# Performance work log

Measured on AMD Instinct MI355X. Metric: run time of the kernel, lower is better.

## Reference

```python
import jax, jax.numpy as jnp
import numpy as np

N = 262144
C = 4096  # number of clusters


def _segment_max(x, seg, num_segments):
    # global_max_pool: per-cluster max over points
    return jax.ops.segment_max(x, seg, num_segments=num_segments)


def setup_inputs() -> dict:
    key = jax.random.key(0)
    ks = jax.random.split(key, 16)

    def lin(k, fan_in, fan_out):
        bound = 1.0 / np.sqrt(fan_in)
        kw, kb = jax.random.split(k)
        W = jax.random.uniform(kw, (fan_in, fan_out), jnp.float32, -bound, bound)
        b = jax.random.uniform(kb, (fan_out,), jnp.float32, -bound, bound)
        return W, b

    relative_points = jax.random.normal(ks[0], (N, 3), jnp.float32)
    features = jax.random.normal(ks[1], (N, 64), jnp.float32)
    cluster = jax.random.randint(ks[2], (N,), 0, C, jnp.int64)

    enc_W1, enc_b1 = lin(ks[3], 3, 32)    # neighborhood encoder MLP
    enc_W2, enc_b2 = lin(ks[4], 32, 64)
    W1, b1 = lin(ks[5], 3 + 64 + 64, 128)  # fc_layers (input_size + enc_out + 3)
    W2, b2 = lin(ks[6], 128, 128)
    G1, gb1 = lin(ks[7], 128, 128)          # fc_layers_global
    G2, gb2 = lin(ks[8], 128, 256)

    return dict(relative_points=relative_points, features=features, cluster=cluster,
                enc_W1=enc_W1, enc_b1=enc_b1, enc_W2=enc_W2, enc_b2=enc_b2,
                W1=W1, b1=b1, W2=W2, b2=b2, G1=G1, gb1=gb1, G2=G2, gb2=gb2)


def reference(relative_points, features, cluster,
              enc_W1, enc_b1, enc_W2, enc_b2,
              W1, b1, W2, b2, G1, gb1, G2, gb2):
    # --- neighborhood encoder: per-point MLP then per-cluster max-pool ---
    h = jax.nn.relu(relative_points @ enc_W1 + enc_b1)          # [N, 32]
    h = jax.nn.relu(h @ enc_W2 + enc_b2)                        # [N, 64]
    neigh_enc = _segment_max(h, cluster, C)                     # [C, 64]

    # gather-by-index duplication + concat
    dup = neigh_enc[cluster]                                    # [N, 64]
    encoded = jnp.concatenate([relative_points, features, dup], axis=1)  # [N, 131]

    # local fc stack (relu, leaky=False)
    encoded = jax.nn.relu(encoded @ W1 + b1)                    # [N, 128]
    encoded = jax.nn.relu(encoded @ W2 + b2)                    # [N, 128]

    # global_max_pool (mean=False)
    encoded_global = _segment_max(encoded, cluster, C)          # [C, 128]

    # global fc stack
    encoded_global = jax.nn.relu(encoded_global @ G1 + gb1)     # [C, 128]
    encoded_global = jax.nn.relu(encoded_global @ G2 + gb2)     # [C, 256]
    return encoded_global
```

## Files before the change

kernel.cpp:

```cpp
#include <hip/hip_runtime.h>
#include <hip/hip_bf16.h>

#define NN 262144
#define CC 4096
#define NBLK 128
#define PPB (NN / NBLK)
#define NT (NN / 64)
#define SLOTS 3

typedef __attribute__((ext_vector_type(8))) short bf16x8;
typedef __attribute__((ext_vector_type(4))) float f32x4;

__device__ __forceinline__ unsigned pk2(float a, float b) {
  __hip_bfloat16 ha = __float2bfloat16(a);
  __hip_bfloat16 hb = __float2bfloat16(b);
  unsigned short ua, ub;
  __builtin_memcpy(&ua, &ha, 2);
  __builtin_memcpy(&ub, &hb, 2);
  return (unsigned)ua | ((unsigned)ub << 16);
}

__global__ __launch_bounds__(256) void k_init(
    const int* __restrict__ cluster, unsigned* __restrict__ hist2d,
    const float* __restrict__ eW2, const float* __restrict__ W1,
    const float* __restrict__ W2, unsigned* __restrict__ packE,
    unsigned* __restrict__ pack1, unsigned* __restrict__ pack2)
{
  __shared__ unsigned h[CC];
  const int t = threadIdx.x, b = blockIdx.x;
  if (b < NBLK) {
    for (int q = t; q < CC; q += 256) h[q] = 0u;
    __syncthreads();
    const int base = b * PPB;
#pragma unroll 4
    for (int k = 0; k < PPB; k += 256) atomicAdd(&h[cluster[base + k + t]], 1u);
    __syncthreads();
    for (int q = t; q < CC; q += 256) hist2d[b * CC + q] = h[q];
    return;
  }
  const int id = (b - NBLK) * 256 + t;
  if (id < 1024) {
    const int nt = id >> 8, l = (id >> 2) & 63, v = id & 3;
    const int k0 = (l >> 4) * 8 + 2 * v, col = nt * 16 + (l & 15);
    packE[id] = pk2(eW2[k0 * 64 + col], eW2[(k0 + 1) * 64 + col]);
  } else if (id < 1024 + 6144) {
    const int j = id - 1024;
    const int kk = j >> 11, nt = (j >> 8) & 7, l = (j >> 2) & 63, v = j & 3;
    const int col = nt * 16 + (l & 15);
    float vals[2];
#pragma unroll
    for (int hh = 0; hh < 2; ++hh) {
      const int k = kk * 32 + (l >> 4) * 8 + 2 * v + hh;
      vals[hh] = (k < 64) ? W1[(3 + k) * 128 + col]
               : (k < 67) ? W1[(k - 64) * 128 + col] : 0.f;
    }
    pack1[j] = pk2(vals[0], vals[1]);
  } else {
    const int j = id - (1024 + 6144);
    const int kk = j >> 11, nt = (j >> 8) & 7, l = (j >> 2) & 63, v = j & 3;
    const int col = nt * 16 + (l & 15);
    const int k0 = kk * 32 + (l >> 4) * 4 + v;
    pack2[j] = pk2(W2[k0 * 128 + col], W2[(k0 + 16) * 128 + col]);
  }
}

__global__ __launch_bounds__(256) void k_scan_a(
    const unsigned* __restrict__ hist2d, unsigned* __restrict__ base2d,
    unsigned* __restrict__ totals)
{
  const int c = blockIdx.x * 256 + threadIdx.x;
  unsigned acc = 0;
#pragma unroll 4
  for (int bb = 0; bb < NBLK; ++bb) {
    const unsigned v = hist2d[bb * CC + c];
    base2d[bb * CC + c] = acc;
    acc += v;
  }
  totals[c] = acc;
}

#define ZERO_F4 589824
__global__ __launch_bounds__(256) void k_scatter(
    const int* __restrict__ cluster, const unsigned* __restrict__ base2d,
    const unsigned* __restrict__ totals, unsigned* __restrict__ permcid,
    unsigned* __restrict__ cstart_g, float4* __restrict__ zbase)
{
  __shared__ unsigned cur[CC];
  __shared__ unsigned part[256];
  const int t = threadIdx.x, b = blockIdx.x;
  if (b >= NBLK) {
    const int zb = b - NBLK;
    const float4 z = {0.f, 0.f, 0.f, 0.f};
#pragma unroll 4
    for (int q = 0; q < 24; ++q)
      zbase[(size_t)(zb * 24 + q) * 256 + t] = z;
    return;
  }
  unsigned loc[16];
  unsigned s = 0;
#pragma unroll
  for (int q = 0; q < 16; ++q) { loc[q] = s; s += totals[t * 16 + q]; }
  part[t] = s;
  __syncthreads();
  for (int off = 1; off < 256; off <<= 1) {
    const unsigned v = (t >= off) ? part[t - off] : 0u;
    __syncthreads();
    part[t] += v;
    __syncthreads();
  }
  const unsigned baset = part[t] - s;
#pragma unroll
  for (int q = 0; q < 16; ++q) {
    const unsigned cs = baset + loc[q];
    cur[t * 16 + q] = base2d[b * CC + t * 16 + q] + cs;
    if (b == 0) cstart_g[t * 16 + q] = cs;
  }
  __syncthreads();
  const int base = b * PPB;
#pragma unroll 4
  for (int k = 0; k < PPB; k += 256) {
    const int i = base + k + t;
    const int c = cluster[i];
    const unsigned pos = atomicAdd(&cur[c], 1u);
    permcid[pos] = (unsigned)i | ((unsigned)c << 18);
  }
}

__global__ __launch_bounds__(256) void k_enc_t(
    const float* __restrict__ pts, const unsigned* __restrict__ permcid,
    const unsigned* __restrict__ cstart,
    const float* __restrict__ eW1, const float* __restrict__ eb1,
    const float* __restrict__ eb2, const unsigned* __restrict__ packE,
    float* __restrict__ pse)
{
  __shared__ float P4[64 * 4];
  __shared__ unsigned h1s[64 * 20];
  __shared__ int seg_r0[65];
  __shared__ int seg_cid[64];
  __shared__ int seg_j[64];
  __shared__ int nseg_s;
  const int t = threadIdx.x;
  const int lane = t & 63, w = t >> 6;
  const int g = lane >> 4, ln15 = lane & 15;
  const int b = blockIdx.x;

  if (w == 0) {
    const unsigned pc = permcid[b * 64 + t];
    const int cid = (int)(pc >> 18);
    const int prevcid = (t == 0) ? -1 : (int)(permcid[b * 64 + t - 1] >> 18);
    const bool flag = (t == 0) || (prevcid != cid);
    const unsigned long long mask = __ballot(flag);
    const int rank = (int)__popcll(mask & ((1ull << t) - 1ull));
    if (flag) {
      seg_r0[rank] = t;
      seg_cid[rank] = cid;
      seg_j[rank] = b - (int)(cstart[cid] >> 6);
    }
    if (t == 0) {
      const int ns = (int)__popcll(mask);
      nseg_s = ns;
      seg_r0[ns] = 64;
    }
    const int i = (int)(pc & 0x3FFFFu);
    P4[t * 4 + 0] = pts[i * 3 + 0];
    P4[t * 4 + 1] = pts[i * 3 + 1];
    P4[t * 4 + 2] = pts[i * 3 + 2];
    P4[t * 4 + 3] = 0.f;
  }
  __syncthreads();
  {
    const int r = t >> 2, qq = t & 3;
    const float p0 = P4[r * 4], p1 = P4[r * 4 + 1], p2 = P4[r * 4 + 2];
    unsigned wv[4];
#pragma unroll
    for (int u = 0; u < 4; ++u) {
      float hv[2];
#pragma unroll
      for (int hh = 0; hh < 2; ++hh) {
        const int cc2 = qq * 8 + 2 * u + hh;
        hv[hh] = fmaxf(fmaf(p2, eW1[64 + cc2],
                       fmaf(p1, eW1[32 + cc2],
                       fmaf(p0, eW1[cc2], eb1[cc2]))), 0.f);
      }
      wv[u] = pk2(hv[0], hv[1]);
    }
    uint4 st; st.x = wv[0]; st.y = wv[1]; st.z = wv[2]; st.w = wv[3];
    *reinterpret_cast<uint4*>(&h1s[r * 20 + qq * 4]) = st;
  }
  __syncthreads();
  {
    const int col = w * 16 + ln15;
    const bf16x8 bfr = *reinterpret_cast<const bf16x8*>(&packE[(w * 64 + lane) * 4]);
    const float bias = eb2[col];
    f32x4 acc[4];
#pragma unroll
    for (int m = 0; m < 4; ++m) acc[m] = f32x4{bias, bias, bias, bias};
#pragma unroll
    for (int m = 0; m < 4; ++m) {
      const bf16x8 a = *reinterpret_cast<const bf16x8*>(&h1s[(16 * m + ln15) * 20 + g * 4]);
      acc[m] = __builtin_amdgcn_mfma_f32_16x16x32_bf16(a, bfr, acc[m], 0, 0, 0);
    }
    const int nseg = nseg_s;
    for (int s = 0; s < nseg; ++s) {
      const int r0 = seg_r0[s], r1 = seg_r0[s + 1];
      float v = 0.f;
#pragma unroll
      for (int m = 0; m < 4; ++m) {
        if (r0 < 16 * (m + 1) && r1 > 16 * m) {
#pragma unroll
          for (int q = 0; q < 4; ++q) {
            const int row = 16 * m + 4 * g + q;
            const bool in = (row >= r0) & (row < r1);
            v = fmaxf(v, in ? acc[m][q] : 0.f);
          }
        }
      }
      v = fmaxf(v, __shfl_xor(v, 16, 64));
      v = fmaxf(v, __shfl_xor(v, 32, 64));
      if (lane < 16) {
        const int c = seg_cid[s], j = seg_j[s];
        if (j < SLOTS - 1)
          pse[((size_t)c * SLOTS + j) * 64 + col] = v;
        else
          atomicMax((int*)&pse[((size_t)c * SLOTS + (SLOTS - 1)) * 64 + col],
                    __float_as_int(v));
      }
    }
  }
}

__global__ __launch_bounds__(256) void k_cproj2(
    const float* __restrict__ pse, const float* __restrict__ W1,
    const float* __restrict__ b1, float* __restrict__ cproj)
{
  __shared__ float nm2[2][64];
  const int t = threadIdx.x, b = blockIdx.x;
  if (t < 128) {
    const int rr = t >> 6, col = t & 63;
    const float* p = pse + ((size_t)(b * 2 + rr) * SLOTS) * 64 + col;
    nm2[rr][col] = fmaxf(fmaxf(p[0], p[64]), p[128]);
  }
  __syncthreads();
  const int rr = t >> 7, col = t & 127;
  const float* __restrict__ Wd = W1 + 67 * 128;
  float a = b1[col];
#pragma unroll 4
  for (int j = 0; j < 16; ++j) {
    const f32x4 nv = *reinterpret_cast<const f32x4*>(&nm2[rr][4 * j]);
    a = fmaf(nv[0], Wd[(4 * j + 0) * 128 + col], a);
    a = fmaf(nv[1], Wd[(4 * j + 1) * 128 + col], a);
    a = fmaf(nv[2], Wd[(4 * j + 2) * 128 + col], a);
    a = fmaf(nv[3], Wd[(4 * j + 3) * 128 + col], a);
  }
  cproj[(size_t)(b * 2 + rr) * 128 + col] = a;
}

__global__ __launch_bounds__(256) void k_fc_t(
    const float* __restrict__ pts, const float* __restrict__ feat,
    const unsigned* __restrict__ permcid, const unsigned* __restrict__ cstart,
    const float* __restrict__ b2, const float* __restrict__ cproj,
    const unsigned* __restrict__ pack1, const unsigned* __restrict__ pack2,
    float* __restrict__ psf)
{
  __shared__ unsigned buf[64 * 68];
  __shared__ int cid_l[64];
  __shared__ int seg_r0[65];
  __shared__ int seg_cid[64];
  __shared__ int seg_j[64];
  __shared__ int nseg_s;
  const int t = threadIdx.x;
  const int lane = t & 63, w = t >> 6;
  const int g = lane >> 4, ln15 = lane & 15;
  const int b = blockIdx.x;

  if (w == 0) {
    const unsigned pc = permcid[b * 64 + t];
    const int cid = (int)(pc >> 18);
    cid_l[t] = cid;
    const int prevcid = (t == 0) ? -1 : (int)(permcid[b * 64 + t - 1] >> 18);
    const bool flag = (t == 0) || (prevcid != cid);
    const unsigned long long mask = __ballot(flag);
    const int rank = (int)__popcll(mask & ((1ull << t) - 1ull));
    if (flag) {
      seg_r0[rank] = t;
      seg_cid[rank] = cid;
      seg_j[rank] = b - (int)(cstart[cid] >> 6);
    }
    if (t == 0) {
      const int ns = (int)__popcll(mask);
      nseg_s = ns;
      seg_r0[ns] = 64;
    }
  }
  {
    const int r = t >> 2, seg = t & 3;
    const int i = (int)(permcid[b * 64 + r] & 0x3FFFFu);
    const float4* __restrict__ fp = reinterpret_cast<const float4*>(&feat[(size_t)i * 64 + seg * 16]);
    const float4 f0 = fp[0], f1 = fp[1], f2 = fp[2], f3 = fp[3];
    uint4 s0v, s1v;
    s0v.x = pk2(f0.x, f0.y); s0v.y = pk2(f0.z, f0.w);
    s0v.z = pk2(f1.x, f1.y); s0v.w = pk2(f1.z, f1.w);
    s1v.x = pk2(f2.x, f2.y); s1v.y = pk2(f2.z, f2.w);
    s1v.z = pk2(f3.x, f3.y); s1v.w = pk2(f3.z, f3.w);
    *reinterpret_cast<uint4*>(&buf[r * 52 + seg * 8 + 0]) = s0v;
    *reinterpret_cast<uint4*>(&buf[r * 52 + seg * 8 + 4]) = s1v;
  }
  if (t < 64) {
    const int i = (int)(permcid[b * 64 + t] & 0x3FFFFu);
    uint4 pw;
    pw.x = pk2(pts[i * 3 + 0], pts[i * 3 + 1]);
    pw.y = pk2(pts[i * 3 + 2], 0.f);
    pw.z = 0u; pw.w = 0u;
    uint4 zz; zz.x = zz.y = zz.z = zz.w = 0u;
    *reinterpret_cast<uint4*>(&buf[t * 52 + 32]) = pw;
    *reinterpret_cast<uint4*>(&buf[t * 52 + 36]) = zz;
    *reinterpret_cast<uint4*>(&buf[t * 52 + 40]) = zz;
    *reinterpret_cast<uint4*>(&buf[t * 52 + 44]) = zz;
  }
  __syncthreads();

  const int colA = w * 32 + ln15, colB = colA + 16;
  f32x4 acc0[4], acc1[4];
  {
#pragma unroll
    for (int m = 0; m < 4; ++m) {
      acc0[m] = f32x4{0.f, 0.f, 0.f, 0.f};
      acc1[m] = f32x4{0.f, 0.f, 0.f, 0.f};
    }
#pragma unroll
    for (int kk = 0; kk < 3; ++kk) {
      const bf16x8 bf0 = *reinterpret_cast<const bf16x8*>(&pack1[((kk * 8 + 2 * w + 0) * 64 + lane) * 4]);
      const bf16x8 bf1 = *reinterpret_cast<const bf16x8*>(&pack1[((kk * 8 + 2 * w + 1) * 64 + lane) * 4]);
#pragma unroll
      for (int m = 0; m < 4; ++m) {
        const bf16x8 a = *reinterpret_cast<const bf16x8*>(&buf[(16 * m + ln15) * 52 + kk * 16 + g * 4]);
        acc0[m] = __builtin_amdgcn_mfma_f32_16x16x32_bf16(a, bf0, acc0[m], 0, 0, 0);
        acc1[m] = __builtin_amdgcn_mfma_f32_16x16x32_bf16(a, bf1, acc1[m], 0, 0, 0);
      }
    }
#pragma unroll
    for (int m = 0; m < 4; ++m)
#pragma unroll
      for (int q = 0; q < 4; ++q) {
        const int row = 16 * m + 4 * g + q;
        const int cc = cid_l[row];
        acc0[m][q] += cproj[(size_t)cc * 128 + colA];
        acc1[m][q] += cproj[(size_t)cc * 128 + colB];
      }
  }
  __syncthreads();
  {
#pragma unroll
    for (int m = 0; m < 4; ++m)
#pragma unroll
      for (int q = 0; q < 4; ++q) {
        const int row = 16 * m + 4 * g + q;
        buf[row * 68 + w * 16 + ln15] =
            pk2(fmaxf(acc0[m][q], 0.f), fmaxf(acc1[m][q], 0.f));
      }
  }
  __syncthreads();
  {
    const float bb0 = b2[colA], bb1 = b2[colB];
#pragma unroll
    for (int m = 0; m < 4; ++m) {
      acc0[m] = f32x4{bb0, bb0, bb0, bb0};
      acc1[m] = f32x4{bb1, bb1, bb1, bb1};
    }
#pragma unroll
    for (int kk = 0; kk < 4; ++kk) {
      const bf16x8 bf0 = *reinterpret_cast<const bf16x8*>(&pack2[((kk * 8 + 2 * w + 0) * 64 + lane) * 4]);
      const bf16x8 bf1 = *reinterpret_cast<const bf16x8*>(&pack2[((kk * 8 + 2 * w + 1) * 64 + lane) * 4]);
#pragma unroll
      for (int m = 0; m < 4; ++m) {
        const bf16x8 a = *reinterpret_cast<const bf16x8*>(&buf[(16 * m + ln15) * 68 + kk * 16 + g * 4]);
        acc0[m] = __builtin_amdgcn_mfma_f32_16x16x32_bf16(a, bf0, acc0[m], 0, 0, 0);
        acc1[m] = __builtin_amdgcn_mfma_f32_16x16x32_bf16(a, bf1, acc1[m], 0, 0, 0);
      }
    }
  }
  {
    const int nseg = nseg_s;
    for (int s = 0; s < nseg; ++s) {
      const int r0 = seg_r0[s], r1 = seg_r0[s + 1];
      float v0 = 0.f, v1 = 0.f;
#pragma unroll
      for (int m = 0; m < 4; ++m) {
        if (r0 < 16 * (m + 1) && r1 > 16 * m) {
#pragma unroll
          for (int q = 0; q < 4; ++q) {
            const int row = 16 * m + 4 * g + q;
            const bool in = (row >= r0) & (row < r1);
            v0 = fmaxf(v0, in ? acc0[m][q] : 0.f);
            v1 = fmaxf(v1, in ? acc1[m][q] : 0.f);
          }
        }
      }
      v0 = fmaxf(v0, __shfl_xor(v0, 16, 64)); v0 = fmaxf(v0, __shfl_xor(v0, 32, 64));
      v1 = fmaxf(v1, __shfl_xor(v1, 16, 64)); v1 = fmaxf(v1, __shfl_xor(v1, 32, 64));
      if (lane < 16) {
        const int c = seg_cid[s], j = seg_j[s];
        if (j < SLOTS - 1) {
          psf[((size_t)c * SLOTS + j) * 128 + colA] = v0;
          psf[((size_t)c * SLOTS + j) * 128 + colB] = v1;
        } else {
          atomicMax((int*)&psf[((size_t)c * SLOTS + (SLOTS - 1)) * 128 + colA], __float_as_int(v0));
          atomicMax((int*)&psf[((size_t)c * SLOTS + (SLOTS - 1)) * 128 + colB], __float_as_int(v1));
        }
      }
    }
  }
}

__global__ __launch_bounds__(256) void k_glob(
    const float* __restrict__ psf, const float* __restrict__ G1,
    const float* __restrict__ gb1, const float* __restrict__ G2,
    const float* __restrict__ gb2, float* __restrict__ out)
{
  __shared__ float pooled[4][128];
  __shared__ float tg[4][128];
  const int t = threadIdx.x, b = blockIdx.x;
  const int c0 = b * 4;
#pragma unroll
  for (int q = 0; q < 2; ++q) {
    const int idx = q * 256 + t;
    const int cc = idx >> 7, col = idx & 127;
    const float* p = psf + (size_t)(c0 + cc) * (SLOTS * 128) + col;
    pooled[cc][col] = fmaxf(fmaxf(p[0], p[128]), p[256]);
  }
  __syncthreads();
  {
    const int col = t & 127, hi = t >> 7;
    float a0 = gb1[col], a1 = a0;
#pragma unroll 4
    for (int k = 0; k < 128; ++k) {
      const float wv = G1[k * 128 + col];
      a0 = fmaf(pooled[hi * 2 + 0][k], wv, a0);
      a1 = fmaf(pooled[hi * 2 + 1][k], wv, a1);
    }
    tg[hi * 2 + 0][col] = fmaxf(a0, 0.f);
    tg[hi * 2 + 1][col] = fmaxf(a1, 0.f);
  }
  __syncthreads();
  {
    float o[4];
#pragma unroll
    for (int q = 0; q < 4; ++q) o[q] = gb2[t];
#pragma unroll 2
    for (int k = 0; k < 128; ++k) {
      const float wv = G2[k * 256 + t];
#pragma unroll
      for (int q = 0; q < 4; ++q) o[q] = fmaf(tg[q][k], wv, o[q]);
    }
#pragma unroll
    for (int q = 0; q < 4; ++q)
      out[(size_t)(c0 + q) * 256 + t] = fmaxf(o[q], 0.f);
  }
}

extern "C" void kernel_launch(void* const* d_in, const int* in_sizes, int n_in,
                              void* d_out, int out_size, void* d_ws, size_t ws_size,
                              hipStream_t stream)
{
  (void)in_sizes; (void)n_in; (void)out_size; (void)ws_size;
  const float* pts  = (const float*)d_in[0];
  const float* feat = (const float*)d_in[1];
  const int*   clus = (const int*)  d_in[2];
  const float* eW1  = (const float*)d_in[3];
  const float* eb1  = (const float*)d_in[4];
  const float* eW2  = (const float*)d_in[5];
  const float* eb2  = (const float*)d_in[6];
  const float* W1   = (const float*)d_in[7];
  const float* b1   = (const float*)d_in[8];
  const float* W2   = (const float*)d_in[9];
  const float* b2   = (const float*)d_in[10];
  const float* G1   = (const float*)d_in[11];
  const float* gb1  = (const float*)d_in[12];
  const float* G2   = (const float*)d_in[13];
  const float* gb2  = (const float*)d_in[14];
  float* out = (float*)d_out;

  unsigned* ws      = (unsigned*)d_ws;
  unsigned* base2d  = ws;
  unsigned* totals  = ws + 524288;
  unsigned* cstart  = ws + 528384;
  unsigned* permcid = ws + 532480;
  unsigned* packE   = ws + 794624;
  unsigned* pack1   = ws + 795648;
  unsigned* pack2   = ws + 801792;
  float*    cproj   = (float*)(ws + 809984);
  float*    pse     = (float*)(ws + 1334272);
  float*    psf     = (float*)(ws + 2120704);
  unsigned* hist2d  = ws + 1334272;

  k_init   <<<NBLK + 60, 256, 0, stream>>>(clus, hist2d, eW2, W1, W2,
                                           packE, pack1, pack2);
  k_scan_a <<<CC / 256, 256, 0, stream>>>(hist2d, base2d, totals);
  k_scatter<<<NBLK + 96, 256, 0, stream>>>(clus, base2d, totals, permcid,
                                           cstart, (float4*)pse);
  k_enc_t  <<<NT, 256, 0, stream>>>(pts, permcid, cstart, eW1, eb1, eb2,
                                    packE, pse);
  k_cproj2 <<<CC / 2, 256, 0, stream>>>(pse, W1, b1, cproj);
  k_fc_t   <<<NT, 256, 0, stream>>>(pts, feat, permcid, cstart, b2, cproj,
                                    pack1, pack2, psf);
  k_glob   <<<1024, 256, 0, stream>>>(psf, G1, gb1, G2, gb2, out);
}
```

Measured before the change: 110.7 us.

## Split fc tile by rows per wave and pool segments through shared memory

Each of the four waves now owns 16 rows of the 64-point tile and computes all 128 output columns, instead of every wave covering all 64 rows for 32 columns. This removes the block-wide barriers between the gather, the first and the second MFMA stages, since each wave reads only its own shared-memory slices. The cost is that every wave now loads the full packed weight fragments. Segment max-pooling becomes a two-step reduction: per-wave partial maxima for up to six segments go to shared memory, then a cross-wave max produces a single store per column. Segments beyond six fall back to per-wave atomicMax into psf.

```diff
diff --git a/kernel.cpp b/kernel.cpp
--- a/kernel.cpp
+++ b/kernel.cpp
@@ -7,6 +7,7 @@
 #define PPB (NN / NBLK)
 #define NT (NN / 64)
 #define SLOTS 3
+#define SMAX 6
 
 typedef __attribute__((ext_vector_type(8))) short bf16x8;
 typedef __attribute__((ext_vector_type(4))) float f32x4;
@@ -79,7 +80,6 @@
   totals[c] = acc;
 }
 
-#define ZERO_F4 589824
 __global__ __launch_bounds__(256) void k_scatter(
     const int* __restrict__ cluster, const unsigned* __restrict__ base2d,
     const unsigned* __restrict__ totals, unsigned* __restrict__ permcid,
@@ -262,8 +262,8 @@
     const unsigned* __restrict__ pack1, const unsigned* __restrict__ pack2,
     float* __restrict__ psf)
 {
-  __shared__ unsigned buf[64 * 68];
-  __shared__ int cid_l[64];
+  __shared__ unsigned xbuf[4 * 16 * 52];
+  __shared__ unsigned e1buf[4 * 16 * 68];
   __shared__ int seg_r0[65];
   __shared__ int seg_cid[64];
   __shared__ int seg_j[64];
@@ -272,11 +272,11 @@
   const int lane = t & 63, w = t >> 6;
   const int g = lane >> 4, ln15 = lane & 15;
   const int b = blockIdx.x;
+  const int wr0 = w * 16;
 
   if (w == 0) {
     const unsigned pc = permcid[b * 64 + t];
     const int cid = (int)(pc >> 18);
-    cid_l[t] = cid;
     const int prevcid = (t == 0) ? -1 : (int)(permcid[b * 64 + t - 1] >> 18);
     const bool flag = (t == 0) || (prevcid != cid);
     const unsigned long long mask = __ballot(flag);
@@ -292,122 +292,139 @@
       seg_r0[ns] = 64;
     }
   }
-  {
-    const int r = t >> 2, seg = t & 3;
-    const int i = (int)(permcid[b * 64 + r] & 0x3FFFFu);
-    const float4* __restrict__ fp = reinterpret_cast<const float4*>(&feat[(size_t)i * 64 + seg * 16]);
+  const int cc0 = (int)(permcid[b * 64 + wr0 + 4 * g + 0] >> 18);
+  const int cc1 = (int)(permcid[b * 64 + wr0 + 4 * g + 1] >> 18);
+  const int cc2 = (int)(permcid[b * 64 + wr0 + 4 * g + 2] >> 18);
+  const int cc3 = (int)(permcid[b * 64 + wr0 + 4 * g + 3] >> 18);
+
+  unsigned* __restrict__ Xw = xbuf + w * 832;
+  {
+    const int r = lane >> 2, sg = lane & 3;
+    const int i = (int)(permcid[b * 64 + wr0 + r] & 0x3FFFFu);
+    const float4* __restrict__ fp = reinterpret_cast<const float4*>(&feat[(size_t)i * 64 + sg * 16]);
     const float4 f0 = fp[0], f1 = fp[1], f2 = fp[2], f3 = fp[3];
     uint4 s0v, s1v;
     s0v.x = pk2(f0.x, f0.y); s0v.y = pk2(f0.z, f0.w);
     s0v.z = pk2(f1.x, f1.y); s0v.w = pk2(f1.z, f1.w);
     s1v.x = pk2(f2.x, f2.y); s1v.y = pk2(f2.z, f2.w);
     s1v.z = pk2(f3.x, f3.y); s1v.w = pk2(f3.z, f3.w);
-    *reinterpret_cast<uint4*>(&buf[r * 52 + seg * 8 + 0]) = s0v;
-    *reinterpret_cast<uint4*>(&buf[r * 52 + seg * 8 + 4]) = s1v;
-  }
-  if (t < 64) {
-    const int i = (int)(permcid[b * 64 + t] & 0x3FFFFu);
-    uint4 pw;
-    pw.x = pk2(pts[i * 3 + 0], pts[i * 3 + 1]);
-    pw.y = pk2(pts[i * 3 + 2], 0.f);
-    pw.z = 0u; pw.w = 0u;
-    uint4 zz; zz.x = zz.y = zz.z = zz.w = 0u;
-    *reinterpret_cast<uint4*>(&buf[t * 52 + 32]) = pw;
-    *reinterpret_cast<uint4*>(&buf[t * 52 + 36]) = zz;
-    *reinterpret_cast<uint4*>(&buf[t * 52 + 40]) = zz;
-    *reinterpret_cast<uint4*>(&buf[t * 52 + 44]) = zz;
-  }
-  __syncthreads();
-
-  const int colA = w * 32 + ln15, colB = colA + 16;
-  f32x4 acc0[4], acc1[4];
-  {
-#pragma unroll
-    for (int m = 0; m < 4; ++m) {
-      acc0[m] = f32x4{0.f, 0.f, 0.f, 0.f};
-      acc1[m] = f32x4{0.f, 0.f, 0.f, 0.f};
-    }
+    *reinterpret_cast<uint4*>(&Xw[r * 52 + sg * 8 + 0]) = s0v;
+    *reinterpret_cast<uint4*>(&Xw[r * 52 + sg * 8 + 4]) = s1v;
+    if (sg == 3) {
+      uint4 pw;
+      pw.x = pk2(pts[i * 3 + 0], pts[i * 3 + 1]);
+      pw.y = pk2(pts[i * 3 + 2], 0.f);
+      pw.z = 0u; pw.w = 0u;
+      uint4 zz; zz.x = zz.y = zz.z = zz.w = 0u;
+      *reinterpret_cast<uint4*>(&Xw[r * 52 + 32]) = pw;
+      *reinterpret_cast<uint4*>(&Xw[r * 52 + 36]) = zz;
+      *reinterpret_cast<uint4*>(&Xw[r * 52 + 40]) = zz;
+      *reinterpret_cast<uint4*>(&Xw[r * 52 + 44]) = zz;
+    }
+  }
+
+  f32x4 acc[8];
+  {
+#pragma unroll
+    for (int nt = 0; nt < 8; ++nt) acc[nt] = f32x4{0.f, 0.f, 0.f, 0.f};
 #pragma unroll
     for (int kk = 0; kk < 3; ++kk) {
-      const bf16x8 bf0 = *reinterpret_cast<const bf16x8*>(&pack1[((kk * 8 + 2 * w + 0) * 64 + lane) * 4]);
-      const bf16x8 bf1 = *reinterpret_cast<const bf16x8*>(&pack1[((kk * 8 + 2 * w + 1) * 64 + lane) * 4]);
-#pragma unroll
-      for (int m = 0; m < 4; ++m) {
-        const bf16x8 a = *reinterpret_cast<const bf16x8*>(&buf[(16 * m + ln15) * 52 + kk * 16 + g * 4]);
-        acc0[m] = __builtin_amdgcn_mfma_f32_16x16x32_bf16(a, bf0, acc0[m], 0, 0, 0);
-        acc1[m] = __builtin_amdgcn_mfma_f32_16x16x32_bf16(a, bf1, acc1[m], 0, 0, 0);
-      }
-    }
-#pragma unroll
-    for (int m = 0; m < 4; ++m)
+      const bf16x8 a = *reinterpret_cast<const bf16x8*>(&Xw[ln15 * 52 + kk * 16 + g * 4]);
+#pragma unroll
+      for (int nt = 0; nt < 8; ++nt) {
+        const bf16x8 bf = *reinterpret_cast<const bf16x8*>(&pack1[((kk * 8 + nt) * 64 + lane) * 4]);
+        acc[nt] = __builtin_amdgcn_mfma_f32_16x16x32_bf16(a, bf, acc[nt], 0, 0, 0);
+      }
+    }
+    const float* __restrict__ cp0 = cproj + (size_t)cc0 * 128 + ln15;
+    const float* __restrict__ cp1 = cproj + (size_t)cc1 * 128 + ln15;
+    const float* __restrict__ cp2 = cproj + (size_t)cc2 * 128 + ln15;
+    const float* __restrict__ cp3 = cproj + (size_t)cc3 * 128 + ln15;
+#pragma unroll
+    for (int nt = 0; nt < 8; ++nt) {
+      acc[nt][0] += cp0[nt * 16];
+      acc[nt][1] += cp1[nt * 16];
+      acc[nt][2] += cp2[nt * 16];
+      acc[nt][3] += cp3[nt * 16];
+    }
+  }
+  unsigned* __restrict__ E1w = e1buf + w * 1088;
+  {
+#pragma unroll
+    for (int u = 0; u < 4; ++u)
+#pragma unroll
+      for (int q = 0; q < 4; ++q)
+        E1w[(4 * g + q) * 68 + u * 16 + ln15] =
+            pk2(fmaxf(acc[2 * u][q], 0.f), fmaxf(acc[2 * u + 1][q], 0.f));
+  }
+  f32x4 o[8];
+  {
+#pragma unroll
+    for (int nt = 0; nt < 8; ++nt) {
+      const float bb = b2[nt * 16 + ln15];
+      o[nt] = f32x4{bb, bb, bb, bb};
+    }
+#pragma unroll
+    for (int kk = 0; kk < 4; ++kk) {
+      const bf16x8 a = *reinterpret_cast<const bf16x8*>(&E1w[ln15 * 68 + kk * 16 + g * 4]);
+#pragma unroll
+      for (int nt = 0; nt < 8; ++nt) {
+        const bf16x8 bf = *reinterpret_cast<const bf16x8*>(&pack2[((kk * 8 + nt) * 64 + lane) * 4]);
+        o[nt] = __builtin_amdgcn_mfma_f32_16x16x32_bf16(a, bf, o[nt], 0, 0, 0);
+      }
+    }
+  }
+  __syncthreads();
+  float* __restrict__ pool = reinterpret_cast<float*>(xbuf);
+  const int nseg = nseg_s;
+  for (int s = 0; s < nseg; ++s) {
+    const int r0 = seg_r0[s], r1 = seg_r0[s + 1];
+    float v[8];
+#pragma unroll
+    for (int nt = 0; nt < 8; ++nt) v[nt] = 0.f;
+    if (r0 < wr0 + 16 && r1 > wr0) {
 #pragma unroll
       for (int q = 0; q < 4; ++q) {
-        const int row = 16 * m + 4 * g + q;
-        const int cc = cid_l[row];
-        acc0[m][q] += cproj[(size_t)cc * 128 + colA];
-        acc1[m][q] += cproj[(size_t)cc * 128 + colB];
-      }
-  }
-  __syncthreads();
-  {
-#pragma unroll
-    for (int m = 0; m < 4; ++m)
-#pragma unroll
-      for (int q = 0; q < 4; ++q) {
-        const int row = 16 * m + 4 * g + q;
-        buf[row * 68 + w * 16 + ln15] =
-            pk2(fmaxf(acc0[m][q], 0.f), fmaxf(acc1[m][q], 0.f));
-      }
-  }
-  __syncthreads();
-  {
-    const float bb0 = b2[colA], bb1 = b2[colB];
-#pragma unroll
-    for (int m = 0; m < 4; ++m) {
-      acc0[m] = f32x4{bb0, bb0, bb0, bb0};
-      acc1[m] = f32x4{bb1, bb1, bb1, bb1};
-    }
-#pragma unroll
-    for (int kk = 0; kk < 4; ++kk) {
-      const bf16x8 bf0 = *reinterpret_cast<const bf16x8*>(&pack2[((kk * 8 + 2 * w + 0) * 64 + lane) * 4]);
-      const bf16x8 bf1 = *reinterpret_cast<const bf16x8*>(&pack2[((kk * 8 + 2 * w + 1) * 64 + lane) * 4]);
-#pragma unroll
-      for (int m = 0; m < 4; ++m) {
-        const bf16x8 a = *reinterpret_cast<const bf16x8*>(&buf[(16 * m + ln15) * 68 + kk * 16 + g * 4]);
-        acc0[m] = __builtin_amdgcn_mfma_f32_16x16x32_bf16(a, bf0, acc0[m], 0, 0, 0);
-        acc1[m] = __builtin_amdgcn_mfma_f32_16x16x32_bf16(a, bf1, acc1[m], 0, 0, 0);
-      }
-    }
-  }
-  {
-    const int nseg = nseg_s;
-    for (int s = 0; s < nseg; ++s) {
-      const int r0 = seg_r0[s], r1 = seg_r0[s + 1];
-      float v0 = 0.f, v1 = 0.f;
-#pragma unroll
-      for (int m = 0; m < 4; ++m) {
-        if (r0 < 16 * (m + 1) && r1 > 16 * m) {
-#pragma unroll
-          for (int q = 0; q < 4; ++q) {
-            const int row = 16 * m + 4 * g + q;
-            const bool in = (row >= r0) & (row < r1);
-            v0 = fmaxf(v0, in ? acc0[m][q] : 0.f);
-            v1 = fmaxf(v1, in ? acc1[m][q] : 0.f);
-          }
-        }
-      }
-      v0 = fmaxf(v0, __shfl_xor(v0, 16, 64)); v0 = fmaxf(v0, __shfl_xor(v0, 32, 64));
-      v1 = fmaxf(v1, __shfl_xor(v1, 16, 64)); v1 = fmaxf(v1, __shfl_xor(v1, 32, 64));
+        const int gr = wr0 + 4 * g + q;
+        const bool in = (gr >= r0) & (gr < r1);
+#pragma unroll
+        for (int nt = 0; nt < 8; ++nt) v[nt] = fmaxf(v[nt], in ? o[nt][q] : 0.f);
+      }
+#pragma unroll
+      for (int nt = 0; nt < 8; ++nt) {
+        v[nt] = fmaxf(v[nt], __shfl_xor(v[nt], 16, 64));
+        v[nt] = fmaxf(v[nt], __shfl_xor(v[nt], 32, 64));
+      }
+    }
+    if (s < SMAX) {
       if (lane < 16) {
-        const int c = seg_cid[s], j = seg_j[s];
-        if (j < SLOTS - 1) {
-          psf[((size_t)c * SLOTS + j) * 128 + colA] = v0;
-          psf[((size_t)c * SLOTS + j) * 128 + colB] = v1;
-        } else {
-          atomicMax((int*)&psf[((size_t)c * SLOTS + (SLOTS - 1)) * 128 + colA], __float_as_int(v0));
-          atomicMax((int*)&psf[((size_t)c * SLOTS + (SLOTS - 1)) * 128 + colB], __float_as_int(v1));
-        }
-      }
+#pragma unroll
+        for (int nt = 0; nt < 8; ++nt)
+          pool[s * 512 + w * 128 + nt * 16 + lane] = v[nt];
+      }
+    } else if (lane < 16) {
+      const int c = seg_cid[s];
+      const int j = seg_j[s];
+      const int jj = (j < SLOTS - 1) ? j : SLOTS - 1;
+#pragma unroll
+      for (int nt = 0; nt < 8; ++nt)
+        atomicMax((int*)&psf[((size_t)c * SLOTS + jj) * 128 + nt * 16 + lane],
+                  __float_as_int(v[nt]));
+    }
+  }
+  __syncthreads();
+  {
+    const int col = t & 127;
+    const int slim = (nseg < SMAX) ? nseg : SMAX;
+    for (int s = t >> 7; s < slim; s += 2) {
+      const float vv = fmaxf(fmaxf(pool[s * 512 + col], pool[s * 512 + 128 + col]),
+                             fmaxf(pool[s * 512 + 256 + col], pool[s * 512 + 384 + col]));
+      const int c = seg_cid[s], j = seg_j[s];
+      if (j < SLOTS - 1)
+        psf[((size_t)c * SLOTS + j) * 128 + col] = vv;
+      else
+        atomicMax((int*)&psf[((size_t)c * SLOTS + (SLOTS - 1)) * 128 + col],
+                  __float_as_int(vv));
     }
   }
 }
```

Measured after the change: 130.7 us. 1.18x slower.

## Process two tiles per block in k_fc_t with prefetched second-tile gathers

Applied to the files above, without the earlier changes.

Each k_fc_t block now handles two 64-row tiles instead of one, halving the grid. Both tiles' feature and point gathers are issued up front so the second tile's global loads overlap the first tile's MFMA work. The point staging is folded into the sg==3 threads instead of a separate wave-0 pass. This raises register pressure from holding the prefetched second tile and reduces the number of blocks available to hide latency.

```diff
diff --git a/kernel.cpp b/kernel.cpp
--- a/kernel.cpp
+++ b/kernel.cpp
@@ -79,7 +79,6 @@
   totals[c] = acc;
 }
 
-#define ZERO_F4 589824
 __global__ __launch_bounds__(256) void k_scatter(
     const int* __restrict__ cluster, const unsigned* __restrict__ base2d,
     const unsigned* __restrict__ totals, unsigned* __restrict__ permcid,
@@ -263,153 +262,191 @@
     float* __restrict__ psf)
 {
   __shared__ unsigned buf[64 * 68];
-  __shared__ int cid_l[64];
-  __shared__ int seg_r0[65];
-  __shared__ int seg_cid[64];
-  __shared__ int seg_j[64];
-  __shared__ int nseg_s;
+  __shared__ int cid_l[2][64];
+  __shared__ int seg_r0[2][65];
+  __shared__ int seg_cid[2][64];
+  __shared__ int seg_j[2][64];
+  __shared__ int nseg_s[2];
   const int t = threadIdx.x;
   const int lane = t & 63, w = t >> 6;
   const int g = lane >> 4, ln15 = lane & 15;
   const int b = blockIdx.x;
 
-  if (w == 0) {
-    const unsigned pc = permcid[b * 64 + t];
+  if (w < 2) {
+    const int tile = 2 * b + w;
+    const unsigned pc = permcid[tile * 64 + lane];
     const int cid = (int)(pc >> 18);
-    cid_l[t] = cid;
-    const int prevcid = (t == 0) ? -1 : (int)(permcid[b * 64 + t - 1] >> 18);
-    const bool flag = (t == 0) || (prevcid != cid);
+    cid_l[w][lane] = cid;
+    const int prevcid = (lane == 0) ? -1 : (int)(permcid[tile * 64 + lane - 1] >> 18);
+    const bool flag = (lane == 0) || (prevcid != cid);
     const unsigned long long mask = __ballot(flag);
-    const int rank = (int)__popcll(mask & ((1ull << t) - 1ull));
+    const int rank = (int)__popcll(mask & ((1ull << lane) - 1ull));
     if (flag) {
-      seg_r0[rank] = t;
-      seg_cid[rank] = cid;
-      seg_j[rank] = b - (int)(cstart[cid] >> 6);
-    }
-    if (t == 0) {
+      seg_r0[w][rank] = lane;
+      seg_cid[w][rank] = cid;
+      seg_j[w][rank] = tile - (int)(cstart[cid] >> 6);
+    }
+    if (lane == 0) {
       const int ns = (int)__popcll(mask);
-      nseg_s = ns;
-      seg_r0[ns] = 64;
-    }
-  }
-  {
-    const int r = t >> 2, seg = t & 3;
-    const int i = (int)(permcid[b * 64 + r] & 0x3FFFFu);
-    const float4* __restrict__ fp = reinterpret_cast<const float4*>(&feat[(size_t)i * 64 + seg * 16]);
-    const float4 f0 = fp[0], f1 = fp[1], f2 = fp[2], f3 = fp[3];
-    uint4 s0v, s1v;
-    s0v.x = pk2(f0.x, f0.y); s0v.y = pk2(f0.z, f0.w);
-    s0v.z = pk2(f1.x, f1.y); s0v.w = pk2(f1.z, f1.w);
-    s1v.x = pk2(f2.x, f2.y); s1v.y = pk2(f2.z, f2.w);
-    s1v.z = pk2(f3.x, f3.y); s1v.w = pk2(f3.z, f3.w);
-    *reinterpret_cast<uint4*>(&buf[r * 52 + seg * 8 + 0]) = s0v;
-    *reinterpret_cast<uint4*>(&buf[r * 52 + seg * 8 + 4]) = s1v;
-  }
-  if (t < 64) {
-    const int i = (int)(permcid[b * 64 + t] & 0x3FFFFu);
-    uint4 pw;
-    pw.x = pk2(pts[i * 3 + 0], pts[i * 3 + 1]);
-    pw.y = pk2(pts[i * 3 + 2], 0.f);
-    pw.z = 0u; pw.w = 0u;
-    uint4 zz; zz.x = zz.y = zz.z = zz.w = 0u;
-    *reinterpret_cast<uint4*>(&buf[t * 52 + 32]) = pw;
-    *reinterpret_cast<uint4*>(&buf[t * 52 + 36]) = zz;
-    *reinterpret_cast<uint4*>(&buf[t * 52 + 40]) = zz;
-    *reinterpret_cast<uint4*>(&buf[t * 52 + 44]) = zz;
-  }
-  __syncthreads();
+      nseg_s[w] = ns;
+      seg_r0[w][ns] = 64;
+    }
+  }
+
+  const int r = t >> 2, sg = t & 3;
+  const int iA = (int)(permcid[(2 * b) * 64 + r] & 0x3FFFFu);
+  const float4* __restrict__ fpA = reinterpret_cast<const float4*>(&feat[(size_t)iA * 64 + sg * 16]);
+  const float4 Af0 = fpA[0], Af1 = fpA[1], Af2 = fpA[2], Af3 = fpA[3];
+  const int iB = (int)(permcid[(2 * b + 1) * 64 + r] & 0x3FFFFu);
+  const float4* __restrict__ fpB = reinterpret_cast<const float4*>(&feat[(size_t)iB * 64 + sg * 16]);
+  const float4 Bf0 = fpB[0], Bf1 = fpB[1], Bf2 = fpB[2], Bf3 = fpB[3];
+  float Ap0 = 0.f, Ap1 = 0.f, Ap2 = 0.f, Bp0 = 0.f, Bp1 = 0.f, Bp2 = 0.f;
+  if (sg == 3) {
+    Ap0 = pts[iA * 3 + 0]; Ap1 = pts[iA * 3 + 1]; Ap2 = pts[iA * 3 + 2];
+    Bp0 = pts[iB * 3 + 0]; Bp1 = pts[iB * 3 + 1]; Bp2 = pts[iB * 3 + 2];
+  }
+
+#define STAGE_X(F0, F1, F2, F3, P0, P1, P2)                                    \
+  {                                                                            \
+    uint4 s0v, s1v;                                                            \
+    s0v.x = pk2(F0.x, F0.y); s0v.y = pk2(F0.z, F0.w);                          \
+    s0v.z = pk2(F1.x, F1.y); s0v.w = pk2(F1.z, F1.w);                          \
+    s1v.x = pk2(F2.x, F2.y); s1v.y = pk2(F2.z, F2.w);                          \
+    s1v.z = pk2(F3.x, F3.y); s1v.w = pk2(F3.z, F3.w);                          \
+    *reinterpret_cast<uint4*>(&buf[r * 52 + sg * 8 + 0]) = s0v;                \
+    *reinterpret_cast<uint4*>(&buf[r * 52 + sg * 8 + 4]) = s1v;                \
+    if (sg == 3) {                                                             \
+      uint4 pw;                                                                \
+      pw.x = pk2(P0, P1); pw.y = pk2(P2, 0.f); pw.z = 0u; pw.w = 0u;           \
+      uint4 zz; zz.x = zz.y = zz.z = zz.w = 0u;                                \
+      *reinterpret_cast<uint4*>(&buf[r * 52 + 32]) = pw;                       \
+      *reinterpret_cast<uint4*>(&buf[r * 52 + 36]) = zz;                       \
+      *reinterpret_cast<uint4*>(&buf[r * 52 + 40]) = zz;                       \
+      *reinterpret_cast<uint4*>(&buf[r * 52 + 44]) = zz;                       \
+    }                                                                          \
+  }
 
   const int colA = w * 32 + ln15, colB = colA + 16;
   f32x4 acc0[4], acc1[4];
-  {
-#pragma unroll
-    for (int m = 0; m < 4; ++m) {
-      acc0[m] = f32x4{0.f, 0.f, 0.f, 0.f};
-      acc1[m] = f32x4{0.f, 0.f, 0.f, 0.f};
-    }
-#pragma unroll
-    for (int kk = 0; kk < 3; ++kk) {
-      const bf16x8 bf0 = *reinterpret_cast<const bf16x8*>(&pack1[((kk * 8 + 2 * w + 0) * 64 + lane) * 4]);
-      const bf16x8 bf1 = *reinterpret_cast<const bf16x8*>(&pack1[((kk * 8 + 2 * w + 1) * 64 + lane) * 4]);
-#pragma unroll
-      for (int m = 0; m < 4; ++m) {
-        const bf16x8 a = *reinterpret_cast<const bf16x8*>(&buf[(16 * m + ln15) * 52 + kk * 16 + g * 4]);
-        acc0[m] = __builtin_amdgcn_mfma_f32_16x16x32_bf16(a, bf0, acc0[m], 0, 0, 0);
-        acc1[m] = __builtin_amdgcn_mfma_f32_16x16x32_bf16(a, bf1, acc1[m], 0, 0, 0);
-      }
-    }
-#pragma unroll
-    for (int m = 0; m < 4; ++m)
-#pragma unroll
-      for (int q = 0; q < 4; ++q) {
-        const int row = 16 * m + 4 * g + q;
-        const int cc = cid_l[row];
-        acc0[m][q] += cproj[(size_t)cc * 128 + colA];
-        acc1[m][q] += cproj[(size_t)cc * 128 + colB];
-      }
-  }
-  __syncthreads();
-  {
-#pragma unroll
-    for (int m = 0; m < 4; ++m)
-#pragma unroll
-      for (int q = 0; q < 4; ++q) {
-        const int row = 16 * m + 4 * g + q;
-        buf[row * 68 + w * 16 + ln15] =
-            pk2(fmaxf(acc0[m][q], 0.f), fmaxf(acc1[m][q], 0.f));
-      }
-  }
-  __syncthreads();
-  {
-    const float bb0 = b2[colA], bb1 = b2[colB];
-#pragma unroll
-    for (int m = 0; m < 4; ++m) {
-      acc0[m] = f32x4{bb0, bb0, bb0, bb0};
-      acc1[m] = f32x4{bb1, bb1, bb1, bb1};
-    }
-#pragma unroll
-    for (int kk = 0; kk < 4; ++kk) {
-      const bf16x8 bf0 = *reinterpret_cast<const bf16x8*>(&pack2[((kk * 8 + 2 * w + 0) * 64 + lane) * 4]);
-      const bf16x8 bf1 = *reinterpret_cast<const bf16x8*>(&pack2[((kk * 8 + 2 * w + 1) * 64 + lane) * 4]);
-#pragma unroll
-      for (int m = 0; m < 4; ++m) {
-        const bf16x8 a = *reinterpret_cast<const bf16x8*>(&buf[(16 * m + ln15) * 68 + kk * 16 + g * 4]);
-        acc0[m] = __builtin_amdgcn_mfma_f32_16x16x32_bf16(a, bf0, acc0[m], 0, 0, 0);
-        acc1[m] = __builtin_amdgcn_mfma_f32_16x16x32_bf16(a, bf1, acc1[m], 0, 0, 0);
-      }
-    }
-  }
-  {
-    const int nseg = nseg_s;
-    for (int s = 0; s < nseg; ++s) {
-      const int r0 = seg_r0[s], r1 = seg_r0[s + 1];
-      float v0 = 0.f, v1 = 0.f;
-#pragma unroll
-      for (int m = 0; m < 4; ++m) {
-        if (r0 < 16 * (m + 1) && r1 > 16 * m) {
-#pragma unroll
-          for (int q = 0; q < 4; ++q) {
-            const int row = 16 * m + 4 * g + q;
-            const bool in = (row >= r0) & (row < r1);
-            v0 = fmaxf(v0, in ? acc0[m][q] : 0.f);
-            v1 = fmaxf(v1, in ? acc1[m][q] : 0.f);
-          }
-        }
-      }
-      v0 = fmaxf(v0, __shfl_xor(v0, 16, 64)); v0 = fmaxf(v0, __shfl_xor(v0, 32, 64));
-      v1 = fmaxf(v1, __shfl_xor(v1, 16, 64)); v1 = fmaxf(v1, __shfl_xor(v1, 32, 64));
-      if (lane < 16) {
-        const int c = seg_cid[s], j = seg_j[s];
-        if (j < SLOTS - 1) {
-          psf[((size_t)c * SLOTS + j) * 128 + colA] = v0;
-          psf[((size_t)c * SLOTS + j) * 128 + colB] = v1;
-        } else {
-          atomicMax((int*)&psf[((size_t)c * SLOTS + (SLOTS - 1)) * 128 + colA], __float_as_int(v0));
-          atomicMax((int*)&psf[((size_t)c * SLOTS + (SLOTS - 1)) * 128 + colB], __float_as_int(v1));
-        }
-      }
-    }
-  }
+
+#define FC1(TI)                                                                \
+  {                                                                            \
+    _Pragma("unroll")                                                          \
+    for (int m = 0; m < 4; ++m) {                                              \
+      acc0[m] = f32x4{0.f, 0.f, 0.f, 0.f};                                     \
+      acc1[m] = f32x4{0.f, 0.f, 0.f, 0.f};                                     \
+    }                                                                          \
+    _Pragma("unroll")                                                          \
+    for (int kk = 0; kk < 3; ++kk) {                                           \
+      const bf16x8 bf0 = *reinterpret_cast<const bf16x8*>(&pack1[((kk * 8 + 2 * w + 0) * 64 + lane) * 4]); \
+      const bf16x8 bf1 = *reinterpret_cast<const bf16x8*>(&pack1[((kk * 8 + 2 * w + 1) * 64 + lane) * 4]); \
+      _Pragma("unroll")                                                        \
+      for (int m = 0; m < 4; ++m) {                                            \
+        const bf16x8 a = *reinterpret_cast<const bf16x8*>(&buf[(16 * m + ln15) * 52 + kk * 16 + g * 4]);   \
+        acc0[m] = __builtin_amdgcn_mfma_f32_16x16x32_bf16(a, bf0, acc0[m], 0, 0, 0); \
+        acc1[m] = __builtin_amdgcn_mfma_f32_16x16x32_bf16(a, bf1, acc1[m], 0, 0, 0); \
+      }                                                                        \
+    }                                                                          \
+    _Pragma("unroll")                                                          \
+    for (int m = 0; m < 4; ++m)                                                \
+      _Pragma("unroll")                                                        \
+      for (int q = 0; q < 4; ++q) {                                            \
+        const int row = 16 * m + 4 * g + q;                                    \
+        const int cc = cid_l[TI][row];                                         \
+        acc0[m][q] += cproj[(size_t)cc * 128 + colA];                          \
+        acc1[m][q] += cproj[(size_t)cc * 128 + colB];                          \
+      }                                                                        \
+  }
+
+#define E1WRITE                                                                \
+  {                                                                            \
+    _Pragma("unroll")                                                          \
+    for (int m = 0; m < 4; ++m)                                                \
+      _Pragma("unroll")                                                        \
+      for (int q = 0; q < 4; ++q) {                                            \
+        const int row = 16 * m + 4 * g + q;                                    \
+        buf[row * 68 + w * 16 + ln15] =                                        \
+            pk2(fmaxf(acc0[m][q], 0.f), fmaxf(acc1[m][q], 0.f));               \
+      }                                                                        \
+  }
+
+#define FC2                                                                    \
+  {                                                                            \
+    const float bb0 = b2[colA], bb1 = b2[colB];                                \
+    _Pragma("unroll")                                                          \
+    for (int m = 0; m < 4; ++m) {                                              \
+      acc0[m] = f32x4{bb0, bb0, bb0, bb0};                                     \
+      acc1[m] = f32x4{bb1, bb1, bb1, bb1};                                     \
+    }                                                                          \
+    _Pragma("unroll")                                                          \
+    for (int kk = 0; kk < 4; ++kk) {                                           \
+      const bf16x8 bf0 = *reinterpret_cast<const bf16x8*>(&pack2[((kk * 8 + 2 * w + 0) * 64 + lane) * 4]); \
+      const bf16x8 bf1 = *reinterpret_cast<const bf16x8*>(&pack2[((kk * 8 + 2 * w + 1) * 64 + lane) * 4]); \
+      _Pragma("unroll")                                                        \
+      for (int m = 0; m < 4; ++m) {                                            \
+        const bf16x8 a = *reinterpret_cast<const bf16x8*>(&buf[(16 * m + ln15) * 68 + kk * 16 + g * 4]);   \
+        acc0[m] = __builtin_amdgcn_mfma_f32_16x16x32_bf16(a, bf0, acc0[m], 0, 0, 0); \
+        acc1[m] = __builtin_amdgcn_mfma_f32_16x16x32_bf16(a, bf1, acc1[m], 0, 0, 0); \
+      }                                                                        \
+    }                                                                          \
+  }
+
+#define POOL(TI)                                                               \
+  {                                                                            \
+    const int nseg = nseg_s[TI];                                               \
+    for (int s = 0; s < nseg; ++s) {                                           \
+      const int r0 = seg_r0[TI][s], r1 = seg_r0[TI][s + 1];                    \
+      float v0 = 0.f, v1 = 0.f;                                                \
+      _Pragma("unroll")                                                        \
+      for (int m = 0; m < 4; ++m) {                                            \
+        if (r0 < 16 * (m + 1) && r1 > 16 * m) {                                \
+          _Pragma("unroll")                                                    \
+          for (int q = 0; q < 4; ++q) {                                        \
+            const int row = 16 * m + 4 * g + q;                                \
+            const bool in = (row >= r0) & (row < r1);                          \
+            v0 = fmaxf(v0, in ? acc0[m][q] : 0.f);                             \
+            v1 = fmaxf(v1, in ? acc1[m][q] : 0.f);                             \
+          }                                                                    \
+        }                                                                      \
+      }                                                                        \
+      v0 = fmaxf(v0, __shfl_xor(v0, 16, 64)); v0 = fmaxf(v0, __shfl_xor(v0, 32, 64)); \
+      v1 = fmaxf(v1, __shfl_xor(v1, 16, 64)); v1 = fmaxf(v1, __shfl_xor(v1, 32, 64)); \
+      if (lane < 16) {                                                         \
+        const int c = seg_cid[TI][s], j = seg_j[TI][s];                        \
+        if (j < SLOTS - 1) {                                                   \
+          psf[((size_t)c * SLOTS + j) * 128 + colA] = v0;                      \
+          psf[((size_t)c * SLOTS + j) * 128 + colB] = v1;                      \
+        } else {                                                               \
+          atomicMax((int*)&psf[((size_t)c * SLOTS + (SLOTS - 1)) * 128 + colA], __float_as_int(v0)); \
+          atomicMax((int*)&psf[((size_t)c * SLOTS + (SLOTS - 1)) * 128 + colB], __float_as_int(v1)); \
+        }                                                                      \
+      }                                                                        \
+    }                                                                          \
+  }
+
+  STAGE_X(Af0, Af1, Af2, Af3, Ap0, Ap1, Ap2)
+  __syncthreads();
+  FC1(0)
+  __syncthreads();
+  E1WRITE
+  __syncthreads();
+  FC2
+  __syncthreads();
+  STAGE_X(Bf0, Bf1, Bf2, Bf3, Bp0, Bp1, Bp2)
+  POOL(0)
+  __syncthreads();
+  FC1(1)
+  __syncthreads();
+  E1WRITE
+  __syncthreads();
+  FC2
+  POOL(1)
+
+#undef STAGE_X
+#undef FC1
+#undef E1WRITE
+#undef FC2
+#undef POOL
 }
 
 __global__ __launch_bounds__(256) void k_glob(
@@ -501,7 +538,7 @@
   k_enc_t  <<<NT, 256, 0, stream>>>(pts, permcid, cstart, eW1, eb1, eb2,
                                     packE, pse);
   k_cproj2 <<<CC / 2, 256, 0, stream>>>(pse, W1, b1, cproj);
-  k_fc_t   <<<NT, 256, 0, stream>>>(pts, feat, permcid, cstart, b2, cproj,
-                                    pack1, pack2, psf);
+  k_fc_t   <<<NT / 2, 256, 0, stream>>>(pts, feat, permcid, cstart, b2, cproj,
+                                        pack1, pack2, psf);
   k_glob   <<<1024, 256, 0, stream>>>(psf, G1, gb1, G2, gb2, out);
 }
```

After: 113.3 us (median of 2 runs). +2.4%, slower.
